# Performance work log

Hardware: AMD Instinct MI355X
Metric: run time of the kernel (lower is better)

The kernel has to match this reference:

```python
import jax, jax.numpy as jnp
import numpy as np

H = 2048
EPS = 1e-12

def setup_inputs() -> dict:
    key = jax.random.key(0)
    ks = jax.random.split(key, 12)
    B, S = 2, 4096
    scale = 1.0 / np.sqrt(H)
    inp = {
        "hidden_states": jax.random.normal(ks[0], (B, S, H), dtype=jnp.float32),
        "token_type_ids": jax.random.randint(ks[1], (B, S), 0, 2, dtype=jnp.int32),
        "ln_gamma": jnp.ones((H,), jnp.float32),
        "ln_beta": jnp.zeros((H,), jnp.float32),
        "tw1": jax.random.uniform(ks[2], (H, H), jnp.float32, -scale, scale),
        "tb1": jnp.zeros((H,), jnp.float32),
        "tw2": jax.random.uniform(ks[3], (H, H), jnp.float32, -scale, scale),
        "tb2": jnp.zeros((H,), jnp.float32),
        "iw1": jax.random.uniform(ks[4], (H, H), jnp.float32, -scale, scale),
        "ib1": jnp.zeros((H,), jnp.float32),
        "iw2": jax.random.uniform(ks[5], (H, H), jnp.float32, -scale, scale),
        "ib2": jnp.zeros((H,), jnp.float32),
    }
    return inp

def _layernorm(x, g, b):
    mu = jnp.mean(x, axis=-1, keepdims=True)
    var = jnp.mean(jnp.square(x - mu), axis=-1, keepdims=True)
    return (x - mu) * jax.lax.rsqrt(var + EPS) * g + b

def _mlp(x, w1, b1, w2, b2):
    # Linear -> exact GELU -> Linear (torch nn.GELU default is erf-based)
    h = jax.nn.gelu(jnp.einsum('bsh,hk->bsk', x, w1) + b1, approximate=False)
    return jnp.einsum('bsk,kh->bsh', h, w2) + b2

def reference(hidden_states, token_type_ids, ln_gamma, ln_beta,
              tw1, tb1, tw2, tb2, iw1, ib1, iw2, ib2):
    xn = _layernorm(hidden_states, ln_gamma, ln_beta)
    text_mask = (token_type_ids == 0)[..., None]   # [B,S,1]
    image_mask = (token_type_ids == 1)[..., None]
    text_out = _mlp(xn, tw1, tb1, tw2, tb2) * text_mask
    image_out = _mlp(xn, iw1, ib1, iw2, ib2) * image_mask
    # dropout is identity in inference / p=0
    return hidden_states + text_out + image_out
```

## Files before the change

### kernel.cpp

```cpp
#include <hip/hip_runtime.h>
#include <hip/hip_bf16.h>


#define H_DIM 2048
#define FULLROWS 8192
#define TAILROWS 512
#define KSPLIT 8

typedef __attribute__((ext_vector_type(8))) short s16x8;
typedef __attribute__((ext_vector_type(4))) float f32x4;
typedef __attribute__((ext_vector_type(4))) int   i32x4;

typedef __attribute__((address_space(1))) const unsigned int gu32;
typedef __attribute__((address_space(3))) unsigned int lu32;
typedef __attribute__((address_space(3))) short lds_s;

__device__ __forceinline__ void load_lds16(const void* g, void* l) {
  __builtin_amdgcn_global_load_lds((gu32*)g, (lu32*)l, 16, 0, 0);
}

__device__ __forceinline__ s16x8 asbf(i32x4 v) {
  union { i32x4 i; s16x8 s; } u; u.i = v; return u.s;
}

__global__ __launch_bounds__(256) void partition_kernel(
    const int* __restrict__ tt, int T, int* __restrict__ ctrl,
    int* __restrict__ pos, int* __restrict__ rowid) {
  __shared__ int psum[256];
  const int tid = threadIdx.x;
  const int npt = T >> 8;
  const int base = tid * npt;
  int cnt = 0;
  for (int i = 0; i < npt; ++i) cnt += (tt[base + i] == 0);
  psum[tid] = cnt;
  __syncthreads();
  for (int off = 1; off < 256; off <<= 1) {
    int v = psum[tid];
    int add = (tid >= off) ? psum[tid - off] : 0;
    __syncthreads();
    psum[tid] = v + add;
    __syncthreads();
  }
  const int Mt = psum[255];
  const int Mt_pad = (Mt + 255) & ~255;
  int tpos = psum[tid] - cnt;
  int ipos = base - tpos;
  for (int i = 0; i < npt; ++i) {
    const int tok = base + i;
    int p;
    if (tt[tok] == 0) p = tpos++;
    else              p = Mt_pad + ipos++;
    pos[tok] = p;
    rowid[p] = tok;
  }
  const int Mi = T - Mt;
  const int Mi_pad = (Mi + 255) & ~255;
  for (int g = Mt + tid; g < Mt_pad; g += 256) rowid[g] = -1;
  for (int g = Mt_pad + Mi + tid; g < Mt_pad + Mi_pad; g += 256) rowid[g] = -1;
  for (int g = Mt_pad + Mi_pad + tid; g < FULLROWS + TAILROWS; g += 256)
    rowid[g] = -1;
  if (tid == 0) {
    ctrl[0] = Mt; ctrl[1] = Mt_pad; ctrl[2] = Mi; ctrl[3] = Mi_pad;
    ctrl[4] = Mt_pad + Mi_pad;
  }
}

__global__ __launch_bounds__(256) void pad_zero_kernel(
    const int* __restrict__ ctrl, __hip_bfloat16* __restrict__ XG) {
  const int Mt = ctrl[0], Mt_pad = ctrl[1], Mi = ctrl[2];
  const int n1 = Mt_pad - Mt;
  const int start2 = Mt_pad + Mi;
  const int b = blockIdx.x;
  int row;
  if (b < n1) row = Mt + b;
  else {
    const int b2 = b - n1;
    if (start2 + b2 >= FULLROWS + TAILROWS) return;
    row = start2 + b2;
  }
  const int4 z = {0, 0, 0, 0};
  *(int4*)(XG + (size_t)row * H_DIM + threadIdx.x * 8) = z;
}

__global__ __launch_bounds__(256) void transpose_to_bf16(
    const float* __restrict__ W, __hip_bfloat16* __restrict__ WT) {
  __shared__ float tile[32][33];
  const int bx = blockIdx.x, by = blockIdx.y;
  const int tid = threadIdx.x;
  const int r = tid >> 3, c4 = (tid & 7) * 4;
  const float4 v = *(const float4*)(W + (size_t)(by * 32 + r) * H_DIM + bx * 32 + c4);
  tile[r][c4 + 0] = v.x; tile[r][c4 + 1] = v.y;
  tile[r][c4 + 2] = v.z; tile[r][c4 + 3] = v.w;
  __syncthreads();
  union { ushort u[4]; ushort4 v4; } pk;
#pragma unroll
  for (int j = 0; j < 4; ++j) {
    __hip_bfloat16 h = __float2bfloat16(tile[c4 + j][r]);
    pk.u[j] = *(const ushort*)&h;
  }
  *(ushort4*)(WT + (size_t)(bx * 32 + r) * H_DIM + by * 32 + c4) = pk.v4;
}

__global__ __launch_bounds__(256) void ln_scatter_kernel(
    const float* __restrict__ X, const float* __restrict__ gamma,
    const float* __restrict__ beta, const int* __restrict__ pos,
    __hip_bfloat16* __restrict__ XG) {
  const int t = blockIdx.x, tid = threadIdx.x;
  const float* row = X + (size_t)t * H_DIM;
  float x[8];
  {
    float4 v0 = *(const float4*)(row + tid * 8);
    float4 v1 = *(const float4*)(row + tid * 8 + 4);
    x[0] = v0.x; x[1] = v0.y; x[2] = v0.z; x[3] = v0.w;
    x[4] = v1.x; x[5] = v1.y; x[6] = v1.z; x[7] = v1.w;
  }
  float s = 0.f, q = 0.f;
#pragma unroll
  for (int j = 0; j < 8; ++j) { s += x[j]; q += x[j] * x[j]; }
#pragma unroll
  for (int off = 32; off > 0; off >>= 1) {
    s += __shfl_down(s, off);
    q += __shfl_down(q, off);
  }
  __shared__ float ls[4], lq[4];
  if ((tid & 63) == 0) { ls[tid >> 6] = s; lq[tid >> 6] = q; }
  __syncthreads();
  const float S = ls[0] + ls[1] + ls[2] + ls[3];
  const float Q = lq[0] + lq[1] + lq[2] + lq[3];
  const float mu = S * (1.0f / H_DIM);
  const float var = Q * (1.0f / H_DIM) - mu * mu;
  const float rstd = rsqrtf(var + 1e-12f);
  const int p = pos[t];
  float4 g0 = *(const float4*)(gamma + tid * 8);
  float4 g1 = *(const float4*)(gamma + tid * 8 + 4);
  float4 b0 = *(const float4*)(beta + tid * 8);
  float4 b1 = *(const float4*)(beta + tid * 8 + 4);
  float g[8] = {g0.x, g0.y, g0.z, g0.w, g1.x, g1.y, g1.z, g1.w};
  float b[8] = {b0.x, b0.y, b0.z, b0.w, b1.x, b1.y, b1.z, b1.w};
  union { ushort u[8]; int4 v; } pk;
#pragma unroll
  for (int j = 0; j < 8; ++j) {
    float y = (x[j] - mu) * rstd * g[j] + b[j];
    __hip_bfloat16 h = __float2bfloat16(y);
    pk.u[j] = *(const ushort*)&h;
  }
  *(int4*)(XG + (size_t)p * H_DIM + tid * 8) = pk.v;
}

#define DSRD(dst, addr, OFF) \
  asm volatile("ds_read_b128 %0, %1 offset:" OFF : "=v"(dst) : "v"(addr))
#define PBAR asm volatile("s_barrier" ::: "memory")
#define SB0  __builtin_amdgcn_sched_barrier(0)
#define LGKM0 do { \
  asm volatile("s_waitcnt lgkmcnt(0)" ::: "memory"); SB0; } while (0)

__device__ __forceinline__ float gelu_exact(float z) {
  return 0.5f * z * (1.0f + erff(z * 0.70710678118654752f));
}

template <int EPI>
__global__ __launch_bounds__(512, 2) void gemmk(
    const __hip_bfloat16* __restrict__ A,
    const __hip_bfloat16* __restrict__ WTt, const __hip_bfloat16* __restrict__ WTi,
    const float* __restrict__ bt, const float* __restrict__ bi,
    const int* __restrict__ ctrl, const int* __restrict__ rowid,
    __hip_bfloat16* __restrict__ Hout,
    const float* __restrict__ resid, float* __restrict__ Out,
    float* __restrict__ pp) {
  constexpr int K = H_DIM;
  const int Mt_pad = ctrl[1];

  __shared__ __align__(16) char smem[131072];
  const unsigned sBase = (unsigned)(uintptr_t)(lds_s*)smem;

  const int tid = threadIdx.x;
  const int w = tid >> 6, l = tid & 63;
  const int bid = blockIdx.x;

  int m0, n0, kbase, ntiles, kp;
  bool partial;
  if (bid < 256) {
    m0 = (bid >> 3) * 256; n0 = (bid & 7) * 256;
    kbase = 0; ntiles = 32; kp = 0; partial = false;
  } else {
    const int tb = bid - 256;
    kp = tb & 7;
    const int posn = tb >> 3;
    n0 = (posn & 7) * 256;
    m0 = FULLROWS + (posn >> 3) * 256;
    kbase = kp * 256; ntiles = 4; partial = true;
  }
  const bool is_text = (m0 < Mt_pad);
  const short* Ag = (const short*)A;
  const short* Bg = (const short*)(is_text ? WTt : WTi);
  const float* bias = is_text ? bt : bi;

  const int wm = w >> 2, wn = w & 3;
  const int srow8 = l >> 3;
  const int sg = (l & 7) ^ srow8;
  const int scol8 = sg * 8;
  const int r16 = l & 15;
  const int r4base = (l >> 4) * 4;

  auto stageA = [&](int bI, int h, int kk) {
#pragma unroll
    for (int c = 0; c < 2; ++c) {
      const short* src = Ag + (size_t)(m0 + h * 128 + c * 64 + w * 8 + srow8) * K + kk + scol8;
      load_lds16(src, smem + bI * 32768 + h * 16384 + (c * 4096 + w * 512) * 2);
    }
  };
  auto stageB = [&](int bI, int h, int kk) {
#pragma unroll
    for (int c = 0; c < 2; ++c) {
      const short* src = Bg + (size_t)(n0 + h * 128 + c * 64 + w * 8 + srow8) * K + kk + scol8;
      load_lds16(src, smem + 65536 + bI * 32768 + h * 16384 + (c * 4096 + w * 512) * 2);
    }
  };

  int off2[2];
#pragma unroll
  for (int ks = 0; ks < 2; ++ks)
    off2[ks] = r16 * 64 + (((ks * 4 + (l >> 4)) ^ (l & 7)) * 8);

  unsigned ardA[2][2], ardB[2][2];
#pragma unroll
  for (int bI = 0; bI < 2; ++bI)
#pragma unroll
    for (int ks = 0; ks < 2; ++ks) {
      ardA[bI][ks] = sBase + bI * 32768u + (unsigned)(wm * 16384 + off2[ks] * 2);
      ardB[bI][ks] = sBase + 65536u + bI * 32768u +
                     (unsigned)((wn >> 1) * 16384 + ((wn & 1) * 4096 + off2[ks]) * 2);
    }

  i32x4 a[4][2], b[4][2];
  f32x4 acc[8][4];
  const f32x4 zero = {0.f, 0.f, 0.f, 0.f};
#pragma unroll
  for (int i = 0; i < 8; ++i)
#pragma unroll
    for (int j = 0; j < 4; ++j) acc[i][j] = zero;

  auto mfmaQ = [&](int fmBase, int fnBase) {
#pragma unroll
    for (int fm = 0; fm < 4; ++fm)
#pragma unroll
      for (int fn = 0; fn < 2; ++fn)
#pragma unroll
        for (int ks = 0; ks < 2; ++ks)
          acc[fmBase + fm][fnBase + fn] = __builtin_amdgcn_mfma_f32_16x16x32_bf16(
              asbf(a[fm][ks]), asbf(b[fnBase + fn][ks]),
              acc[fmBase + fm][fnBase + fn], 0, 0, 0);
  };

#define TILE(C) do {                                                          \
    DSRD(a[0][0], ardA[C][0], "0");     DSRD(a[0][1], ardA[C][1], "0");       \
    DSRD(a[1][0], ardA[C][0], "2048");  DSRD(a[1][1], ardA[C][1], "2048");    \
    DSRD(a[2][0], ardA[C][0], "4096");  DSRD(a[2][1], ardA[C][1], "4096");    \
    DSRD(a[3][0], ardA[C][0], "6144");  DSRD(a[3][1], ardA[C][1], "6144");    \
    DSRD(b[0][0], ardB[C][0], "0");     DSRD(b[0][1], ardB[C][1], "0");       \
    DSRD(b[1][0], ardB[C][0], "2048");  DSRD(b[1][1], ardB[C][1], "2048");    \
    stageA(C ^ 1, 0, _kA);                                                    \
    PBAR; LGKM0;                                                              \
    __builtin_amdgcn_s_setprio(1); mfmaQ(0, 0); __builtin_amdgcn_s_setprio(0);\
    SB0; PBAR;                                                                \
    DSRD(b[2][0], ardB[C][0], "4096");  DSRD(b[2][1], ardB[C][1], "4096");    \
    DSRD(b[3][0], ardB[C][0], "6144");  DSRD(b[3][1], ardB[C][1], "6144");    \
    stageA(C ^ 1, 1, _kA);                                                    \
    PBAR; LGKM0;                                                              \
    __builtin_amdgcn_s_setprio(1); mfmaQ(0, 2); __builtin_amdgcn_s_setprio(0);\
    SB0; PBAR;                                                                \
    DSRD(a[0][0], ardA[C][0], "8192");  DSRD(a[0][1], ardA[C][1], "8192");    \
    DSRD(a[1][0], ardA[C][0], "10240"); DSRD(a[1][1], ardA[C][1], "10240");   \
    DSRD(a[2][0], ardA[C][0], "12288"); DSRD(a[2][1], ardA[C][1], "12288");   \
    DSRD(a[3][0], ardA[C][0], "14336"); DSRD(a[3][1], ardA[C][1], "14336");   \
    stageB(C, 0, _kB);                                                        \
    PBAR; LGKM0;                                                              \
    __builtin_amdgcn_s_setprio(1); mfmaQ(4, 2); __builtin_amdgcn_s_setprio(0);\
    SB0; PBAR;                                                                \
    stageB(C, 1, _kB);                                                        \
    asm volatile("s_waitcnt vmcnt(4)" ::: "memory");                          \
    PBAR; SB0;                                                                \
    __builtin_amdgcn_s_setprio(1); mfmaQ(4, 0); __builtin_amdgcn_s_setprio(0);\
    SB0; PBAR;                                                                \
  } while (0)

  stageA(0, 0, kbase); stageA(0, 1, kbase);
  stageB(0, 0, kbase); stageB(0, 1, kbase);
  stageB(1, 0, kbase + 64); stageB(1, 1, kbase + 64);
  asm volatile("s_waitcnt vmcnt(4)" ::: "memory");
  PBAR;

  int _kA, _kB;
  for (int t = 0; t < ntiles; t += 2) {
    _kA = kbase + (t + 1 < ntiles ? t + 1 : ntiles - 1) * 64;
    _kB = kbase + (t + 2 < ntiles ? t + 2 : ntiles - 1) * 64;
    TILE(0);
    _kA = kbase + (t + 2 < ntiles ? t + 2 : ntiles - 1) * 64;
    _kB = kbase + (t + 3 < ntiles ? t + 3 : ntiles - 1) * 64;
    TILE(1);
  }
#undef TILE
  asm volatile("s_waitcnt vmcnt(0) lgkmcnt(0)" ::: "memory");

  if (!partial) {
    float bb[4];
#pragma unroll
    for (int fn = 0; fn < 4; ++fn) bb[fn] = bias[n0 + wn * 64 + fn * 16 + r16];
    if (EPI == 0) {
#pragma unroll
      for (int fm = 0; fm < 8; ++fm) {
        const int grow = m0 + wm * 128 + fm * 16 + r4base;
#pragma unroll
        for (int fn = 0; fn < 4; ++fn) {
          const int gcol = n0 + wn * 64 + fn * 16 + r16;
          f32x4 v = acc[fm][fn];
#pragma unroll
          for (int i = 0; i < 4; ++i)
            Hout[(size_t)(grow + i) * K + gcol] = __float2bfloat16(gelu_exact(v[i] + bb[fn]));
        }
      }
    } else {
#pragma unroll
      for (int fm = 0; fm < 8; ++fm) {
        const int grow = m0 + wm * 128 + fm * 16 + r4base;
        int rid[4];
#pragma unroll
        for (int i = 0; i < 4; ++i) rid[i] = rowid[grow + i];
#pragma unroll
        for (int fn = 0; fn < 4; ++fn) {
          const int gcol = n0 + wn * 64 + fn * 16 + r16;
          f32x4 v = acc[fm][fn];
#pragma unroll
          for (int i = 0; i < 4; ++i) {
            if (rid[i] >= 0) {
              const size_t o = (size_t)rid[i] * K + gcol;
              Out[o] = resid[o] + v[i] + bb[fn];
            }
          }
        }
      }
    }
  } else {
    float* ppk = pp + (size_t)kp * TAILROWS * H_DIM;
    const int mrel = m0 - FULLROWS;
#pragma unroll
    for (int fm = 0; fm < 8; ++fm) {
      const int prow = mrel + wm * 128 + fm * 16 + r4base;
#pragma unroll
      for (int fn = 0; fn < 4; ++fn) {
        const int gcol = n0 + wn * 64 + fn * 16 + r16;
        f32x4 v = acc[fm][fn];
#pragma unroll
        for (int i = 0; i < 4; ++i)
          ppk[(size_t)(prow + i) * H_DIM + gcol] = v[i];
      }
    }
  }
}

template <int EPI>
__global__ __launch_bounds__(256) void combine_kernel(
    const float* __restrict__ pp, const float* __restrict__ bt,
    const float* __restrict__ bi, const int* __restrict__ ctrl,
    const int* __restrict__ rowid, __hip_bfloat16* __restrict__ Hout,
    const float* __restrict__ resid, float* __restrict__ Out) {
  const int u = blockIdx.x * 256 + threadIdx.x;
  const int r = u >> 9;
  const int c = (u & 511) * 4;
  const size_t off = (size_t)r * H_DIM + c;
  float4 s = *(const float4*)(pp + off);
#pragma unroll
  for (int k = 1; k < KSPLIT; ++k) {
    const float4 sk = *(const float4*)(pp + (size_t)k * TAILROWS * H_DIM + off);
    s.x += sk.x; s.y += sk.y; s.z += sk.z; s.w += sk.w;
  }
  const int grow = FULLROWS + r;
  const float* bias = (grow < ctrl[1]) ? bt : bi;
  const float4 bb = *(const float4*)(bias + c);
  if (EPI == 0) {
    union { ushort u4[4]; ushort4 v4; } pk;
    float z[4] = {s.x + bb.x, s.y + bb.y, s.z + bb.z, s.w + bb.w};
#pragma unroll
    for (int j = 0; j < 4; ++j) {
      __hip_bfloat16 h = __float2bfloat16(0.5f * z[j] * (1.0f + erff(z[j] * 0.70710678118654752f)));
      pk.u4[j] = *(const ushort*)&h;
    }
    *(ushort4*)(Hout + (size_t)grow * H_DIM + c) = pk.v4;
  } else {
    const int rid = rowid[grow];
    if (rid >= 0) {
      const size_t o = (size_t)rid * H_DIM + c;
      const float4 rv = *(const float4*)(resid + o);
      float4 ov;
      ov.x = rv.x + s.x + bb.x; ov.y = rv.y + s.y + bb.y;
      ov.z = rv.z + s.z + bb.z; ov.w = rv.w + s.w + bb.w;
      *(float4*)(Out + o) = ov;
    }
  }
}

extern "C" void kernel_launch(void* const* d_in, const int* in_sizes, int n_in,
                              void* d_out, int out_size, void* d_ws, size_t ws_size,
                              hipStream_t stream) {
  const float* hidden = (const float*)d_in[0];
  const int*   tt     = (const int*)d_in[1];
  const float* gamma  = (const float*)d_in[2];
  const float* beta   = (const float*)d_in[3];
  const float* tw1    = (const float*)d_in[4];
  const float* tb1    = (const float*)d_in[5];
  const float* tw2    = (const float*)d_in[6];
  const float* tb2    = (const float*)d_in[7];
  const float* iw1    = (const float*)d_in[8];
  const float* ib1    = (const float*)d_in[9];
  const float* iw2    = (const float*)d_in[10];
  const float* ib2    = (const float*)d_in[11];
  float* out = (float*)d_out;

  const int T = in_sizes[1];
  const int K = H_DIM;
  const int maxrows = FULLROWS + TAILROWS;

  char* ws = (char*)d_ws;
  int* ctrl  = (int*)(ws);
  int* pos   = (int*)(ws + 4096);
  int* rowid = (int*)(ws + 65536);
  const size_t WOFF = 131072;
  const size_t WSZ = (size_t)K * K * sizeof(__hip_bfloat16);
  __hip_bfloat16* wTs0 = (__hip_bfloat16*)(ws + WOFF);
  __hip_bfloat16* wTs1 = (__hip_bfloat16*)(ws + WOFF + WSZ);
  __hip_bfloat16* xg   = (__hip_bfloat16*)(ws + WOFF + 2 * WSZ);
  __hip_bfloat16* hb   = xg + (size_t)maxrows * K;
  float* pp = (float*)(hb + (size_t)maxrows * K);

  partition_kernel<<<1, 256, 0, stream>>>(tt, T, ctrl, pos, rowid);
  pad_zero_kernel<<<512, 256, 0, stream>>>(ctrl, xg);

  dim3 tg(K / 32, K / 32);
  transpose_to_bf16<<<tg, 256, 0, stream>>>(tw1, wTs0);
  transpose_to_bf16<<<tg, 256, 0, stream>>>(iw1, wTs1);

  ln_scatter_kernel<<<T, 256, 0, stream>>>(hidden, gamma, beta, pos, xg);

  gemmk<0><<<384, 512, 0, stream>>>(xg, wTs0, wTs1, tb1, ib1, ctrl, rowid,
                                    hb, nullptr, nullptr, pp);
  combine_kernel<0><<<1024, 256, 0, stream>>>(pp, tb1, ib1, ctrl, rowid,
                                              hb, nullptr, nullptr);

  transpose_to_bf16<<<tg, 256, 0, stream>>>(tw2, wTs0);
  transpose_to_bf16<<<tg, 256, 0, stream>>>(iw2, wTs1);

  gemmk<1><<<384, 512, 0, stream>>>(hb, wTs0, wTs1, tb2, ib2, ctrl, rowid,
                                    nullptr, hidden, out, pp);
  combine_kernel<1><<<1024, 256, 0, stream>>>(pp, tb2, ib2, ctrl, rowid,
                                              nullptr, hidden, out);
}
```

Before: 272.3 us.

## Reduce barriers in GEMM pipeline, specialize full/partial paths, merge transpose launches

The GEMM tile macro is restructured to issue both halves of the A and B staging loads together and to drop several workgroup barriers, merging the last two MFMA quarters into one block. The full-K and split-K tail paths now each get their own code with a compile-time loop count and a fully unrolled four-tile sequence. The two weight transposes per layer are merged into one launch using a z-grid dimension. The aim is less barrier stall and launch overhead, at the cost of fewer sync points, which risks LDS read/write hazards and changes the overlap of loads with MFMAs.

```diff
diff --git a/kernel.cpp b/kernel.cpp
--- a/kernel.cpp
+++ b/kernel.cpp
@@ -82,10 +82,13 @@
   *(int4*)(XG + (size_t)row * H_DIM + threadIdx.x * 8) = z;
 }
 
-__global__ __launch_bounds__(256) void transpose_to_bf16(
-    const float* __restrict__ W, __hip_bfloat16* __restrict__ WT) {
+__global__ __launch_bounds__(256) void transpose_to_bf16_x2(
+    const float* __restrict__ W0, const float* __restrict__ W1,
+    __hip_bfloat16* __restrict__ O0, __hip_bfloat16* __restrict__ O1) {
   __shared__ float tile[32][33];
-  const int bx = blockIdx.x, by = blockIdx.y;
+  const int bx = blockIdx.x, by = blockIdx.y, bz = blockIdx.z;
+  const float* W = (bz == 0) ? W0 : W1;
+  __hip_bfloat16* WT = (bz == 0) ? O0 : O1;
   const int tid = threadIdx.x;
   const int r = tid >> 3, c4 = (tid & 7) * 4;
   const float4 v = *(const float4*)(W + (size_t)(by * 32 + r) * H_DIM + bx * 32 + c4);
@@ -177,45 +180,12 @@
   const int w = tid >> 6, l = tid & 63;
   const int bid = blockIdx.x;
 
-  int m0, n0, kbase, ntiles, kp;
-  bool partial;
-  if (bid < 256) {
-    m0 = (bid >> 3) * 256; n0 = (bid & 7) * 256;
-    kbase = 0; ntiles = 32; kp = 0; partial = false;
-  } else {
-    const int tb = bid - 256;
-    kp = tb & 7;
-    const int posn = tb >> 3;
-    n0 = (posn & 7) * 256;
-    m0 = FULLROWS + (posn >> 3) * 256;
-    kbase = kp * 256; ntiles = 4; partial = true;
-  }
-  const bool is_text = (m0 < Mt_pad);
-  const short* Ag = (const short*)A;
-  const short* Bg = (const short*)(is_text ? WTt : WTi);
-  const float* bias = is_text ? bt : bi;
-
-  const int wm = w >> 2, wn = w & 3;
   const int srow8 = l >> 3;
   const int sg = (l & 7) ^ srow8;
   const int scol8 = sg * 8;
   const int r16 = l & 15;
   const int r4base = (l >> 4) * 4;
-
-  auto stageA = [&](int bI, int h, int kk) {
-#pragma unroll
-    for (int c = 0; c < 2; ++c) {
-      const short* src = Ag + (size_t)(m0 + h * 128 + c * 64 + w * 8 + srow8) * K + kk + scol8;
-      load_lds16(src, smem + bI * 32768 + h * 16384 + (c * 4096 + w * 512) * 2);
-    }
-  };
-  auto stageB = [&](int bI, int h, int kk) {
-#pragma unroll
-    for (int c = 0; c < 2; ++c) {
-      const short* src = Bg + (size_t)(n0 + h * 128 + c * 64 + w * 8 + srow8) * K + kk + scol8;
-      load_lds16(src, smem + 65536 + bI * 32768 + h * 16384 + (c * 4096 + w * 512) * 2);
-    }
-  };
+  const int wm = w >> 2, wn = w & 3;
 
   int off2[2];
 #pragma unroll
@@ -259,50 +229,70 @@
     DSRD(a[3][0], ardA[C][0], "6144");  DSRD(a[3][1], ardA[C][1], "6144");    \
     DSRD(b[0][0], ardB[C][0], "0");     DSRD(b[0][1], ardB[C][1], "0");       \
     DSRD(b[1][0], ardB[C][0], "2048");  DSRD(b[1][1], ardB[C][1], "2048");    \
-    stageA(C ^ 1, 0, _kA);                                                    \
-    PBAR; LGKM0;                                                              \
+    stageA(C ^ 1, 0, _kA); stageA(C ^ 1, 1, _kA);                             \
+    LGKM0;                                                                    \
     __builtin_amdgcn_s_setprio(1); mfmaQ(0, 0); __builtin_amdgcn_s_setprio(0);\
-    SB0; PBAR;                                                                \
+    SB0;                                                                      \
     DSRD(b[2][0], ardB[C][0], "4096");  DSRD(b[2][1], ardB[C][1], "4096");    \
     DSRD(b[3][0], ardB[C][0], "6144");  DSRD(b[3][1], ardB[C][1], "6144");    \
-    stageA(C ^ 1, 1, _kA);                                                    \
-    PBAR; LGKM0;                                                              \
+    LGKM0;                                                                    \
     __builtin_amdgcn_s_setprio(1); mfmaQ(0, 2); __builtin_amdgcn_s_setprio(0);\
-    SB0; PBAR;                                                                \
+    SB0;                                                                      \
     DSRD(a[0][0], ardA[C][0], "8192");  DSRD(a[0][1], ardA[C][1], "8192");    \
     DSRD(a[1][0], ardA[C][0], "10240"); DSRD(a[1][1], ardA[C][1], "10240");   \
     DSRD(a[2][0], ardA[C][0], "12288"); DSRD(a[2][1], ardA[C][1], "12288");   \
     DSRD(a[3][0], ardA[C][0], "14336"); DSRD(a[3][1], ardA[C][1], "14336");   \
-    stageB(C, 0, _kB);                                                        \
     PBAR; LGKM0;                                                              \
-    __builtin_amdgcn_s_setprio(1); mfmaQ(4, 2); __builtin_amdgcn_s_setprio(0);\
-    SB0; PBAR;                                                                \
-    stageB(C, 1, _kB);                                                        \
+    stageB(C, 0, _kB); stageB(C, 1, _kB);                                     \
+    SB0;                                                                      \
+    __builtin_amdgcn_s_setprio(1); mfmaQ(4, 2); mfmaQ(4, 0);                  \
+    __builtin_amdgcn_s_setprio(0);                                            \
+    SB0;                                                                      \
     asm volatile("s_waitcnt vmcnt(4)" ::: "memory");                          \
-    PBAR; SB0;                                                                \
-    __builtin_amdgcn_s_setprio(1); mfmaQ(4, 0); __builtin_amdgcn_s_setprio(0);\
-    SB0; PBAR;                                                                \
+    PBAR;                                                                     \
   } while (0)
 
-  stageA(0, 0, kbase); stageA(0, 1, kbase);
-  stageB(0, 0, kbase); stageB(0, 1, kbase);
-  stageB(1, 0, kbase + 64); stageB(1, 1, kbase + 64);
-  asm volatile("s_waitcnt vmcnt(4)" ::: "memory");
-  PBAR;
-
-  int _kA, _kB;
-  for (int t = 0; t < ntiles; t += 2) {
-    _kA = kbase + (t + 1 < ntiles ? t + 1 : ntiles - 1) * 64;
-    _kB = kbase + (t + 2 < ntiles ? t + 2 : ntiles - 1) * 64;
-    TILE(0);
-    _kA = kbase + (t + 2 < ntiles ? t + 2 : ntiles - 1) * 64;
-    _kB = kbase + (t + 3 < ntiles ? t + 3 : ntiles - 1) * 64;
-    TILE(1);
-  }
-#undef TILE
-  asm volatile("s_waitcnt vmcnt(0) lgkmcnt(0)" ::: "memory");
-
-  if (!partial) {
+  if (bid < 256) {
+    constexpr int NT = K / 64;
+    const int m0 = (bid >> 3) * 256;
+    const int n0 = (bid & 7) * 256;
+    const bool is_text = (m0 < Mt_pad);
+    const short* Ag = (const short*)A;
+    const short* Bg = (const short*)(is_text ? WTt : WTi);
+    const float* bias = is_text ? bt : bi;
+
+    auto stageA = [&](int bI, int h, int kk) {
+#pragma unroll
+      for (int c = 0; c < 2; ++c) {
+        const short* src = Ag + (size_t)(m0 + h * 128 + c * 64 + w * 8 + srow8) * K + kk + scol8;
+        load_lds16(src, smem + bI * 32768 + h * 16384 + (c * 4096 + w * 512) * 2);
+      }
+    };
+    auto stageB = [&](int bI, int h, int kk) {
+#pragma unroll
+      for (int c = 0; c < 2; ++c) {
+        const short* src = Bg + (size_t)(n0 + h * 128 + c * 64 + w * 8 + srow8) * K + kk + scol8;
+        load_lds16(src, smem + 65536 + bI * 32768 + h * 16384 + (c * 4096 + w * 512) * 2);
+      }
+    };
+
+    stageA(0, 0, 0); stageA(0, 1, 0);
+    stageB(0, 0, 0); stageB(0, 1, 0);
+    stageB(1, 0, 64); stageB(1, 1, 64);
+    asm volatile("s_waitcnt vmcnt(4)" ::: "memory");
+    PBAR;
+
+    int _kA, _kB;
+    for (int t = 0; t < NT; t += 2) {
+      _kA = (t + 1 < NT ? t + 1 : NT - 1) * 64;
+      _kB = (t + 2 < NT ? t + 2 : NT - 1) * 64;
+      TILE(0);
+      _kA = (t + 2 < NT ? t + 2 : NT - 1) * 64;
+      _kB = (t + 3 < NT ? t + 3 : NT - 1) * 64;
+      TILE(1);
+    }
+    asm volatile("s_waitcnt vmcnt(0) lgkmcnt(0)" ::: "memory");
+
     float bb[4];
 #pragma unroll
     for (int fn = 0; fn < 4; ++fn) bb[fn] = bias[n0 + wn * 64 + fn * 16 + r16];
@@ -341,6 +331,44 @@
       }
     }
   } else {
+    const int tb = bid - 256;
+    const int kp = tb & 7;
+    const int posn = tb >> 3;
+    const int n0 = (posn & 7) * 256;
+    const int m0 = FULLROWS + (posn >> 3) * 256;
+    const int kb = kp * 256;
+    const bool is_text = (m0 < Mt_pad);
+    const short* Ag = (const short*)A;
+    const short* Bg = (const short*)(is_text ? WTt : WTi);
+
+    auto stageA = [&](int bI, int h, int kk) {
+#pragma unroll
+      for (int c = 0; c < 2; ++c) {
+        const short* src = Ag + (size_t)(m0 + h * 128 + c * 64 + w * 8 + srow8) * K + kk + scol8;
+        load_lds16(src, smem + bI * 32768 + h * 16384 + (c * 4096 + w * 512) * 2);
+      }
+    };
+    auto stageB = [&](int bI, int h, int kk) {
+#pragma unroll
+      for (int c = 0; c < 2; ++c) {
+        const short* src = Bg + (size_t)(n0 + h * 128 + c * 64 + w * 8 + srow8) * K + kk + scol8;
+        load_lds16(src, smem + 65536 + bI * 32768 + h * 16384 + (c * 4096 + w * 512) * 2);
+      }
+    };
+
+    stageA(0, 0, kb); stageA(0, 1, kb);
+    stageB(0, 0, kb); stageB(0, 1, kb);
+    stageB(1, 0, kb + 64); stageB(1, 1, kb + 64);
+    asm volatile("s_waitcnt vmcnt(4)" ::: "memory");
+    PBAR;
+
+    int _kA, _kB;
+    _kA = kb + 64;  _kB = kb + 128;  TILE(0);
+    _kA = kb + 128; _kB = kb + 192;  TILE(1);
+    _kA = kb + 192; _kB = kb + 192;  TILE(0);
+    _kA = kb + 192; _kB = kb + 192;  TILE(1);
+    asm volatile("s_waitcnt vmcnt(0) lgkmcnt(0)" ::: "memory");
+
     float* ppk = pp + (size_t)kp * TAILROWS * H_DIM;
     const int mrel = m0 - FULLROWS;
 #pragma unroll
@@ -356,6 +384,7 @@
       }
     }
   }
+#undef TILE
 }
 
 template <int EPI>
@@ -435,9 +464,8 @@
   partition_kernel<<<1, 256, 0, stream>>>(tt, T, ctrl, pos, rowid);
   pad_zero_kernel<<<512, 256, 0, stream>>>(ctrl, xg);
 
-  dim3 tg(K / 32, K / 32);
-  transpose_to_bf16<<<tg, 256, 0, stream>>>(tw1, wTs0);
-  transpose_to_bf16<<<tg, 256, 0, stream>>>(iw1, wTs1);
+  dim3 tg(K / 32, K / 32, 2);
+  transpose_to_bf16_x2<<<tg, 256, 0, stream>>>(tw1, iw1, wTs0, wTs1);
 
   ln_scatter_kernel<<<T, 256, 0, stream>>>(hidden, gamma, beta, pos, xg);
 
@@ -446,8 +474,7 @@
   combine_kernel<0><<<1024, 256, 0, stream>>>(pp, tb1, ib1, ctrl, rowid,
                                               hb, nullptr, nullptr);
 
-  transpose_to_bf16<<<tg, 256, 0, stream>>>(tw2, wTs0);
-  transpose_to_bf16<<<tg, 256, 0, stream>>>(iw2, wTs1);
+  transpose_to_bf16_x2<<<tg, 256, 0, stream>>>(tw2, iw2, wTs0, wTs1);
 
   gemmk<1><<<384, 512, 0, stream>>>(hb, wTs0, wTs1, tb2, ib2, ctrl, rowid,
                                     nullptr, hidden, out, pp);
```

After: 267.8 us. About the same (-1.6%).
